# Kernel optimization log

Hardware: AMD Instinct MI355X
Metric: run time of the kernel (lower is better)

Reference implementation:

```python
import math
import jax, jax.numpy as jnp
import numpy as np

B, S, D = 4, 2048, 1024
NEG = -1e20

def setup_inputs() -> dict:
    key = jax.random.key(0)
    k1, k2, k3, k4 = jax.random.split(key, 4)
    X = jax.random.normal(k1, (B, S, D), dtype=jnp.float32)
    # True = masked position (masked_fill semantics)
    attention_mask = jax.random.randint(k2, (B, S, S), 0, 2).astype(bool)
    scale = 1.0 / math.sqrt(D)
    W_qkv = jax.random.normal(k3, (D, 3 * D), dtype=jnp.float32) * scale
    b_qkv = jnp.zeros((3 * D,), dtype=jnp.float32)
    W_out = jax.random.normal(k4, (D, D), dtype=jnp.float32) * scale
    b_out = jnp.zeros((D,), dtype=jnp.float32)
    return {"X": X, "attention_mask": attention_mask,
            "W_qkv": W_qkv, "b_qkv": b_qkv, "W_out": W_out, "b_out": b_out}

def reference(X, attention_mask, W_qkv, b_qkv, W_out, b_out):
    dim = X.shape[-1]
    QKV = X @ W_qkv + b_qkv                      # [B,S,3D]
    Q, K, V = jnp.split(QKV, 3, axis=-1)         # each [B,S,D]
    scores = jnp.einsum('bqd,bkd->bqk', Q, K) / math.sqrt(dim)  # [B,S,S]
    scores = jnp.where(attention_mask, NEG, scores)
    attn = jax.nn.softmax(scores, axis=-1)       # dropout_rate=0.0 -> identity
    ctx = jnp.einsum('bqk,bkd->bqd', attn, V)    # [B,S,D]
    return ctx @ W_out + b_out
```

## Files before the change

### kernel.cpp

```cpp
#include <hip/hip_runtime.h>
#include <cstdint>
#include <cstddef>

#define BB 4
#define SS 2048
#define DD 1024

typedef _Float16 f16;
typedef _Float16 f16x8 __attribute__((ext_vector_type(8)));
typedef _Float16 f16x4 __attribute__((ext_vector_type(4)));
typedef float fx4 __attribute__((ext_vector_type(4)));

__device__ __forceinline__ void async_copy16(void* lds, const void* g) {
  __builtin_amdgcn_global_load_lds(
      (__attribute__((address_space(1))) void*)const_cast<void*>(g),
      (__attribute__((address_space(3))) void*)lds,
      16, 0, 0);
}

enum { EPI_BIAS = 0, EPI_MASKEXP = 1, EPI_ROWSCALE = 2, EPI_QKV = 3 };

template <typename OutT, int MODE>
__global__ __launch_bounds__(256, 2) void gemm_nt(
    const f16* __restrict__ A, long long strideA, int lda,
    const f16* __restrict__ Bt, long long strideB, int ldb,
    OutT* __restrict__ C, long long strideC, int ldc,
    const float* __restrict__ bias, const int* __restrict__ mask,
    float* __restrict__ rowSum, f16* __restrict__ vt, float scale, int K) {
  constexpr int SMEM_BYTES = (MODE == EPI_MASKEXP) ? 34816 : 32768;
  __shared__ __align__(16) char smem[SMEM_BYTES];
  uint32_t* lmb = (uint32_t*)(smem + 32768);

  const int t = threadIdx.x;
  const int lane = t & 63;
  const int wid = t >> 6;
  const long long bz = blockIdx.z;
  const int tileM = blockIdx.y * 128;
  const int tileN = blockIdx.x * 128;

  const f16* Ab = A + bz * strideA;
  const f16* Bb = Bt + bz * strideB;
  OutT* Cb = C + bz * strideC;

  const int sr = t >> 2;
  const int sc = (((t & 3) ^ ((t >> 3) & 3)) * 8);
  const f16* pa0 = Ab + (size_t)(tileM + sr) * lda + sc;
  const f16* pa1 = Ab + (size_t)(tileM + 64 + sr) * lda + sc;
  const f16* pb0 = Bb + (size_t)(tileN + sr) * ldb + sc;
  const f16* pb1 = Bb + (size_t)(tileN + 64 + sr) * ldb + sc;
  const int tb = t * 16;

  const int waveM = (wid >> 1) * 64;
  const int waveN = (wid & 1) * 64;
  const int r16 = lane & 15;
  const int quad = lane >> 4;
  const int sw = (r16 >> 1) & 3;

  if constexpr (MODE == EPI_MASKEXP) {
    const int* maskb = mask + bz * (long long)SS * SS;
#pragma unroll
    for (int it = 0; it < 16; ++it) {
      const int f = it * 256 + t;
      const int4 mv =
          *(const int4*)&maskb[(size_t)(tileM + (f >> 5)) * SS + tileN + (f & 31) * 4];
      uint32_t val = (mv.x ? 1u : 0u) | (mv.y ? 2u : 0u) | (mv.z ? 4u : 0u) |
                     (mv.w ? 8u : 0u);
      val <<= (t & 7) * 4;
      val |= __shfl_xor(val, 1, 64);
      val |= __shfl_xor(val, 2, 64);
      val |= __shfl_xor(val, 4, 64);
      if ((t & 7) == 0) lmb[it * 32 + (t >> 3)] = val;
    }
    __syncthreads();
  }

  const int nIter = K >> 5;
  {
    char* b0 = smem;
    async_copy16(b0 + tb, pa0);
    async_copy16(b0 + 4096 + tb, pa1);
    async_copy16(b0 + 8192 + tb, pb0);
    async_copy16(b0 + 12288 + tb, pb1);
  }

  fx4 acc[4][4] = {};

#pragma unroll 2
  for (int i = 0; i < nIter; ++i) {
    __syncthreads();
    if (i + 1 < nIter) {
      char* nb = smem + ((i + 1) & 1) * 16384;
      const int k = (i + 1) << 5;
      async_copy16(nb + tb, pa0 + k);
      async_copy16(nb + 4096 + tb, pa1 + k);
      async_copy16(nb + 8192 + tb, pb0 + k);
      async_copy16(nb + 12288 + tb, pb1 + k);
    }
    const f16* As = (const f16*)(smem + (i & 1) * 16384);
    const f16* Bs = As + 4096;

    f16x8 af[4], bf[4];
#pragma unroll
    for (int x = 0; x < 4; ++x)
      af[x] = *(const f16x8*)&As[(waveM + x * 16 + r16) * 32 + (quad ^ sw) * 8];
#pragma unroll
    for (int x = 0; x < 4; ++x)
      bf[x] = *(const f16x8*)&Bs[(waveN + x * 16 + r16) * 32 + (quad ^ sw) * 8];

#pragma unroll
    for (int x = 0; x < 4; ++x)
#pragma unroll
      for (int j = 0; j < 4; ++j)
        acc[x][j] =
            __builtin_amdgcn_mfma_f32_16x16x32_f16(af[x], bf[j], acc[x][j], 0, 0, 0);
  }

  if constexpr (MODE == EPI_BIAS) {
#pragma unroll
    for (int j = 0; j < 4; ++j) {
      const int col = tileN + waveN + j * 16 + r16;
      const float bv = bias[col];
#pragma unroll
      for (int i = 0; i < 4; ++i) {
#pragma unroll
        for (int r = 0; r < 4; ++r) {
          const int row = tileM + waveM + i * 16 + quad * 4 + r;
          Cb[(size_t)row * ldc + col] = (OutT)(acc[i][j][r] * scale + bv);
        }
      }
    }
  } else if constexpr (MODE == EPI_QKV) {
    if (tileN < 2 * DD) {
#pragma unroll
      for (int j = 0; j < 4; ++j) {
        const int col = tileN + waveN + j * 16 + r16;
        const float bv = bias[col];
#pragma unroll
        for (int i = 0; i < 4; ++i) {
#pragma unroll
          for (int r = 0; r < 4; ++r) {
            const int row = tileM + waveM + i * 16 + quad * 4 + r;
            Cb[(size_t)row * ldc + col] = (OutT)(acc[i][j][r] + bv);
          }
        }
      }
    } else {
      const int b = tileM >> 11;
      const int s0 = (tileM & 2047) + waveM;
      f16* vb = vt + (size_t)b * DD * SS;
#pragma unroll
      for (int j = 0; j < 4; ++j) {
        const int col = tileN + waveN + j * 16 + r16;
        const float bv = bias[col];
        const int d = col - 2 * DD;
#pragma unroll
        for (int i = 0; i < 4; ++i) {
          const int s = s0 + i * 16 + quad * 4;
          f16x4 v4;
#pragma unroll
          for (int r = 0; r < 4; ++r) v4[r] = (f16)(acc[i][j][r] + bv);
          *(f16x4*)&vb[(size_t)d * SS + s] = v4;
        }
      }
    }
  } else if constexpr (MODE == EPI_MASKEXP) {
#pragma unroll
    for (int i = 0; i < 4; ++i) {
#pragma unroll
      for (int r = 0; r < 4; ++r) {
        const int lr = waveM + i * 16 + quad * 4 + r;
        const int row = tileM + lr;
        const uint32_t w0 = lmb[lr * 4 + (waveN >> 5)];
        const uint32_t w1 = lmb[lr * 4 + (waveN >> 5) + 1];
        float part = 0.0f;
#pragma unroll
        for (int j = 0; j < 4; ++j) {
          const int lc = waveN + j * 16 + r16;
          const int bitpos = j * 16 + r16;
          const uint32_t mv = ((j < 2 ? w0 : w1) >> (bitpos & 31)) & 1u;
          const float e = mv ? 0.0f : __expf(acc[i][j][r] * scale);
          Cb[(size_t)row * ldc + tileN + lc] = (OutT)e;
          part += e;
        }
#pragma unroll
        for (int d = 1; d < 16; d <<= 1) part += __shfl_xor(part, d, 64);
        if (r16 == 0) atomicAdd(&rowSum[bz * SS + row], part);
      }
    }
  } else {
#pragma unroll
    for (int i = 0; i < 4; ++i) {
#pragma unroll
      for (int r = 0; r < 4; ++r) {
        const int row = tileM + waveM + i * 16 + quad * 4 + r;
        const float inv = scale / rowSum[bz * SS + row];
#pragma unroll
        for (int j = 0; j < 4; ++j) {
          const int col = tileN + waveN + j * 16 + r16;
          Cb[(size_t)row * ldc + col] = (OutT)(acc[i][j][r] * inv);
        }
      }
    }
  }
}

__global__ __launch_bounds__(256) void k_prep(
    const float* __restrict__ X, f16* __restrict__ Xh,
    const float* __restrict__ Wqkv, f16* __restrict__ Wqkvt,
    const float* __restrict__ Wout, f16* __restrict__ Woutt,
    float* __restrict__ rowSum) {
  int bid = blockIdx.x;
  const int t = threadIdx.x;
  if (bid < 8192) {
    const int i = bid * 256 + t;
    const float4 v = ((const float4*)X)[i];
    f16x4 h = {(f16)v.x, (f16)v.y, (f16)v.z, (f16)v.w};
    ((f16x4*)Xh)[i] = h;
    return;
  }
  bid -= 8192;
  __shared__ float tile[32][33];
  const int tx = t & 31, ty = t >> 5;
  if (bid < 3072) {
    const int bx = (bid % 96) * 32, by = (bid / 96) * 32;
    for (int i2 = ty; i2 < 32; i2 += 8)
      tile[i2][tx] = Wqkv[(size_t)(by + i2) * 3072 + bx + tx];
    __syncthreads();
    for (int i2 = ty; i2 < 32; i2 += 8)
      Wqkvt[(size_t)(bx + i2) * 1024 + by + tx] = (f16)tile[tx][i2];
    return;
  }
  bid -= 3072;
  if (bid < 1024) {
    const int bx = (bid & 31) * 32, by = (bid >> 5) * 32;
    for (int i2 = ty; i2 < 32; i2 += 8)
      tile[i2][tx] = Wout[(size_t)(by + i2) * 1024 + bx + tx];
    __syncthreads();
    for (int i2 = ty; i2 < 32; i2 += 8)
      Woutt[(size_t)(bx + i2) * 1024 + by + tx] = (f16)tile[tx][i2];
    return;
  }
  bid -= 1024;
  rowSum[bid * 256 + t] = 0.0f;
}

extern "C" void kernel_launch(void* const* d_in, const int* in_sizes, int n_in,
                              void* d_out, int out_size, void* d_ws, size_t ws_size,
                              hipStream_t stream) {
  const float* X = (const float*)d_in[0];
  const int* mask = (const int*)d_in[1];
  const float* Wqkv = (const float*)d_in[2];
  const float* bqkv = (const float*)d_in[3];
  const float* Wout = (const float*)d_in[4];
  const float* bout = (const float*)d_in[5];
  float* out = (float*)d_out;

  char* ws = (char*)d_ws;
  f16* Xh = (f16*)(ws + 0);
  f16* Wqkvt = (f16*)(ws + 16777216);
  f16* Woutt = (f16*)(ws + 23068672);
  f16* QK = (f16*)(ws + 25165824);
  f16* Vt = (f16*)(ws + 58720256);
  f16* E = (f16*)(ws + 75497472);
  f16* Ctx = (f16*)(ws + 109051904);
  float* rowSum = (float*)(ws + 125829120);

  k_prep<<<dim3(12320), dim3(256), 0, stream>>>(X, Xh, Wqkv, Wqkvt, Wout, Woutt,
                                                rowSum);

  gemm_nt<f16, EPI_QKV><<<dim3(24, 64, 1), dim3(256), 0, stream>>>(
      Xh, 0LL, DD, Wqkvt, 0LL, DD, QK, 0LL, 2 * DD, bqkv, nullptr, nullptr, Vt,
      1.0f, DD);

  gemm_nt<f16, EPI_MASKEXP><<<dim3(16, 16, 4), dim3(256), 0, stream>>>(
      QK, (long long)SS * 2 * DD, 2 * DD, QK + DD, (long long)SS * 2 * DD, 2 * DD,
      E, (long long)SS * SS, SS, nullptr, mask, rowSum, nullptr, 0.03125f, DD);

  gemm_nt<f16, EPI_ROWSCALE><<<dim3(8, 16, 4), dim3(256), 0, stream>>>(
      E, (long long)SS * SS, SS, Vt, (long long)DD * SS, SS, Ctx,
      (long long)SS * DD, DD, nullptr, nullptr, rowSum, nullptr, 1.0f, SS);

  gemm_nt<float, EPI_BIAS><<<dim3(8, 64, 1), dim3(256), 0, stream>>>(
      Ctx, 0LL, DD, Woutt, 0LL, DD, out, 0LL, DD, bout, nullptr, nullptr, nullptr,
      1.0f, DD);
}
```

Baseline: 338.2 us.

## Use 256x256 eight-wave GEMM tiles with ping-pong LDS schedule and prepacked mask bits

The GEMM grows from 128x128 tiles with 4 waves to 256x256 tiles with 8 waves. Each wave now holds a 128x64 accumulator, and K-steps of 64 are double-buffered in 128KB of LDS, with explicit barriers, waitcnt and setprio interleaving loads with MFMA bursts. The aim is more data reuse per LDS byte and better overlap of copies with math. The int mask is packed into bitmasks once in the prep kernel, stored in a workspace region that aliases the Ctx buffer, and read directly in the epilogue, so the per-tile mask staging is gone. The risk is that the smaller grids (128 blocks for two of the GEMMs) and one block per CU may leave many CUs idle.

```diff
diff --git a/kernel.cpp b/kernel.cpp
--- a/kernel.cpp
+++ b/kernel.cpp
@@ -21,98 +21,124 @@
 enum { EPI_BIAS = 0, EPI_MASKEXP = 1, EPI_ROWSCALE = 2, EPI_QKV = 3 };
 
 template <typename OutT, int MODE>
-__global__ __launch_bounds__(256, 2) void gemm_nt(
+__global__ __launch_bounds__(512, 2) void gemm_nt8(
     const f16* __restrict__ A, long long strideA, int lda,
     const f16* __restrict__ Bt, long long strideB, int ldb,
     OutT* __restrict__ C, long long strideC, int ldc,
-    const float* __restrict__ bias, const int* __restrict__ mask,
+    const float* __restrict__ bias, const uint32_t* __restrict__ gmask,
     float* __restrict__ rowSum, f16* __restrict__ vt, float scale, int K) {
-  constexpr int SMEM_BYTES = (MODE == EPI_MASKEXP) ? 34816 : 32768;
-  __shared__ __align__(16) char smem[SMEM_BYTES];
-  uint32_t* lmb = (uint32_t*)(smem + 32768);
+  __shared__ __align__(16) char smem[131072];
 
   const int t = threadIdx.x;
   const int lane = t & 63;
   const int wid = t >> 6;
   const long long bz = blockIdx.z;
-  const int tileM = blockIdx.y * 128;
-  const int tileN = blockIdx.x * 128;
+  const int tileM = blockIdx.y * 256;
+  const int tileN = blockIdx.x * 256;
 
   const f16* Ab = A + bz * strideA;
   const f16* Bb = Bt + bz * strideB;
   OutT* Cb = C + bz * strideC;
 
-  const int sr = t >> 2;
-  const int sc = (((t & 3) ^ ((t >> 3) & 3)) * 8);
-  const f16* pa0 = Ab + (size_t)(tileM + sr) * lda + sc;
-  const f16* pa1 = Ab + (size_t)(tileM + 64 + sr) * lda + sc;
-  const f16* pb0 = Bb + (size_t)(tileN + sr) * ldb + sc;
-  const f16* pb1 = Bb + (size_t)(tileN + 64 + sr) * ldb + sc;
+  const int gch = ((t & 3) ^ ((t >> 3) & 3)) * 8;
+  const f16* pA = Ab + (size_t)(tileM + (t >> 2)) * lda + gch;
+  const f16* pB = Bb + (size_t)(tileN + (t >> 2)) * ldb + gch;
+  const size_t rA = (size_t)128 * lda;
+  const size_t rB = (size_t)128 * ldb;
   const int tb = t * 16;
 
-  const int waveM = (wid >> 1) * 64;
-  const int waveN = (wid & 1) * 64;
+  const int waveM = (wid >> 2) * 128;
+  const int waveN = (wid & 3) * 64;
   const int r16 = lane & 15;
   const int quad = lane >> 4;
   const int sw = (r16 >> 1) & 3;
 
-  if constexpr (MODE == EPI_MASKEXP) {
-    const int* maskb = mask + bz * (long long)SS * SS;
-#pragma unroll
-    for (int it = 0; it < 16; ++it) {
-      const int f = it * 256 + t;
-      const int4 mv =
-          *(const int4*)&maskb[(size_t)(tileM + (f >> 5)) * SS + tileN + (f & 31) * 4];
-      uint32_t val = (mv.x ? 1u : 0u) | (mv.y ? 2u : 0u) | (mv.z ? 4u : 0u) |
-                     (mv.w ? 8u : 0u);
-      val <<= (t & 7) * 4;
-      val |= __shfl_xor(val, 1, 64);
-      val |= __shfl_xor(val, 2, 64);
-      val |= __shfl_xor(val, 4, 64);
-      if ((t & 7) == 0) lmb[it * 32 + (t >> 3)] = val;
-    }
-    __syncthreads();
-  }
-
-  const int nIter = K >> 5;
-  {
-    char* b0 = smem;
-    async_copy16(b0 + tb, pa0);
-    async_copy16(b0 + 4096 + tb, pa1);
-    async_copy16(b0 + 8192 + tb, pb0);
-    async_copy16(b0 + 12288 + tb, pb1);
-  }
-
-  fx4 acc[4][4] = {};
-
-#pragma unroll 2
-  for (int i = 0; i < nIter; ++i) {
-    __syncthreads();
-    if (i + 1 < nIter) {
-      char* nb = smem + ((i + 1) & 1) * 16384;
-      const int k = (i + 1) << 5;
-      async_copy16(nb + tb, pa0 + k);
-      async_copy16(nb + 4096 + tb, pa1 + k);
-      async_copy16(nb + 8192 + tb, pb0 + k);
-      async_copy16(nb + 12288 + tb, pb1 + k);
-    }
-    const f16* As = (const f16*)(smem + (i & 1) * 16384);
-    const f16* Bs = As + 4096;
-
-    f16x8 af[4], bf[4];
-#pragma unroll
-    for (int x = 0; x < 4; ++x)
-      af[x] = *(const f16x8*)&As[(waveM + x * 16 + r16) * 32 + (quad ^ sw) * 8];
-#pragma unroll
-    for (int x = 0; x < 4; ++x)
-      bf[x] = *(const f16x8*)&Bs[(waveN + x * 16 + r16) * 32 + (quad ^ sw) * 8];
-
-#pragma unroll
-    for (int x = 0; x < 4; ++x)
-#pragma unroll
-      for (int j = 0; j < 4; ++j)
-        acc[x][j] =
-            __builtin_amdgcn_mfma_f32_16x16x32_f16(af[x], bf[j], acc[x][j], 0, 0, 0);
+  const int nT = K >> 6;
+
+#define STG_A(par, ks, Tn)                                      \
+  {                                                             \
+    char* d_ = smem + (par) * 65536 + (ks) * 16384;             \
+    const f16* s_ = pA + (size_t)(Tn) * 64 + (ks) * 32;         \
+    async_copy16(d_ + tb, s_);                                  \
+    async_copy16(d_ + 8192 + tb, s_ + rA);                      \
+  }
+#define STG_B(par, ks, Tn)                                      \
+  {                                                             \
+    char* d_ = smem + (par) * 65536 + 32768 + (ks) * 16384;     \
+    const f16* s_ = pB + (size_t)(Tn) * 64 + (ks) * 32;         \
+    async_copy16(d_ + tb, s_);                                  \
+    async_copy16(d_ + 8192 + tb, s_ + rB);                      \
+  }
+
+  STG_A(0, 0, 0);
+  STG_B(0, 0, 0);
+  STG_A(0, 1, 0);
+  STG_B(0, 1, 0);
+  asm volatile("s_waitcnt vmcnt(4)" ::: "memory");
+  __builtin_amdgcn_s_barrier();
+  __builtin_amdgcn_sched_barrier(0);
+
+  fx4 acc[8][4] = {};
+  f16x8 af[4], bf[4];
+
+#define LOADB(Bs)                                                              \
+  _Pragma("unroll") for (int j = 0; j < 4; ++j) bf[j] =                        \
+      *(const f16x8*)&(Bs)[(waveN + j * 16 + r16) * 32 + (quad ^ sw) * 8];
+#define LOADA(As, mo)                                                          \
+  _Pragma("unroll") for (int m = 0; m < 4; ++m) af[m] =                        \
+      *(const f16x8*)&(As)[(waveM + (mo) + m * 16 + r16) * 32 + (quad ^ sw) * 8];
+#define MFMA16(mo)                                                             \
+  __builtin_amdgcn_s_setprio(1);                                               \
+  _Pragma("unroll") for (int m = 0; m < 4; ++m)                                \
+  _Pragma("unroll") for (int j = 0; j < 4; ++j)                                \
+      acc[(mo) + m][j] = __builtin_amdgcn_mfma_f32_16x16x32_f16(               \
+          af[m], bf[j], acc[(mo) + m][j], 0, 0, 0);                            \
+  __builtin_amdgcn_s_setprio(0);
+
+  for (int T = 0; T < nT; ++T) {
+    const int par = T & 1;
+    const int np = par ^ 1;
+    const bool st = (T + 1) < nT;
+    const f16* As0 = (const f16*)(smem + par * 65536);
+    const f16* As1 = As0 + 8192;
+    const f16* Bs0 = As0 + 16384;
+    const f16* Bs1 = As0 + 24576;
+
+    LOADB(Bs0);
+    LOADA(As0, 0);
+    if (st) STG_A(np, 0, T + 1);
+    __builtin_amdgcn_s_barrier();
+    MFMA16(0);
+    __builtin_amdgcn_s_barrier();
+
+    LOADA(As0, 64);
+    if (st) STG_B(np, 0, T + 1);
+    __builtin_amdgcn_s_barrier();
+    MFMA16(4);
+    if (st) {
+      asm volatile("s_waitcnt vmcnt(4)" ::: "memory");
+    } else {
+      asm volatile("s_waitcnt vmcnt(0)" ::: "memory");
+    }
+    __builtin_amdgcn_s_barrier();
+    __builtin_amdgcn_sched_barrier(0);
+
+    LOADB(Bs1);
+    LOADA(As1, 0);
+    if (st) STG_A(np, 1, T + 1);
+    __builtin_amdgcn_s_barrier();
+    MFMA16(0);
+    __builtin_amdgcn_s_barrier();
+
+    LOADA(As1, 64);
+    if (st) STG_B(np, 1, T + 1);
+    __builtin_amdgcn_s_barrier();
+    MFMA16(4);
+    if (st) {
+      asm volatile("s_waitcnt vmcnt(4)" ::: "memory");
+    }
+    __builtin_amdgcn_s_barrier();
+    __builtin_amdgcn_sched_barrier(0);
   }
 
   if constexpr (MODE == EPI_BIAS) {
@@ -121,11 +147,11 @@
       const int col = tileN + waveN + j * 16 + r16;
       const float bv = bias[col];
 #pragma unroll
-      for (int i = 0; i < 4; ++i) {
+      for (int m = 0; m < 8; ++m) {
 #pragma unroll
         for (int r = 0; r < 4; ++r) {
-          const int row = tileM + waveM + i * 16 + quad * 4 + r;
-          Cb[(size_t)row * ldc + col] = (OutT)(acc[i][j][r] * scale + bv);
+          const int row = tileM + waveM + m * 16 + quad * 4 + r;
+          Cb[(size_t)row * ldc + col] = (OutT)(acc[m][j][r] * scale + bv);
         }
       }
     }
@@ -136,11 +162,11 @@
         const int col = tileN + waveN + j * 16 + r16;
         const float bv = bias[col];
 #pragma unroll
-        for (int i = 0; i < 4; ++i) {
+        for (int m = 0; m < 8; ++m) {
 #pragma unroll
           for (int r = 0; r < 4; ++r) {
-            const int row = tileM + waveM + i * 16 + quad * 4 + r;
-            Cb[(size_t)row * ldc + col] = (OutT)(acc[i][j][r] + bv);
+            const int row = tileM + waveM + m * 16 + quad * 4 + r;
+            Cb[(size_t)row * ldc + col] = (OutT)(acc[m][j][r] + bv);
           }
         }
       }
@@ -154,32 +180,31 @@
         const float bv = bias[col];
         const int d = col - 2 * DD;
 #pragma unroll
-        for (int i = 0; i < 4; ++i) {
-          const int s = s0 + i * 16 + quad * 4;
+        for (int m = 0; m < 8; ++m) {
+          const int s = s0 + m * 16 + quad * 4;
           f16x4 v4;
 #pragma unroll
-          for (int r = 0; r < 4; ++r) v4[r] = (f16)(acc[i][j][r] + bv);
+          for (int r = 0; r < 4; ++r) v4[r] = (f16)(acc[m][j][r] + bv);
           *(f16x4*)&vb[(size_t)d * SS + s] = v4;
         }
       }
     }
   } else if constexpr (MODE == EPI_MASKEXP) {
 #pragma unroll
-    for (int i = 0; i < 4; ++i) {
+    for (int m = 0; m < 8; ++m) {
 #pragma unroll
       for (int r = 0; r < 4; ++r) {
-        const int lr = waveM + i * 16 + quad * 4 + r;
-        const int row = tileM + lr;
-        const uint32_t w0 = lmb[lr * 4 + (waveN >> 5)];
-        const uint32_t w1 = lmb[lr * 4 + (waveN >> 5) + 1];
+        const int row = tileM + waveM + m * 16 + quad * 4 + r;
+        const uint32_t* gr =
+            gmask + (((size_t)bz * SS + row) << 6) + ((tileN + waveN) >> 5);
+        const uint32_t w0 = gr[0], w1 = gr[1];
         float part = 0.0f;
 #pragma unroll
         for (int j = 0; j < 4; ++j) {
-          const int lc = waveN + j * 16 + r16;
           const int bitpos = j * 16 + r16;
           const uint32_t mv = ((j < 2 ? w0 : w1) >> (bitpos & 31)) & 1u;
-          const float e = mv ? 0.0f : __expf(acc[i][j][r] * scale);
-          Cb[(size_t)row * ldc + tileN + lc] = (OutT)e;
+          const float e = mv ? 0.0f : __expf(acc[m][j][r] * scale);
+          Cb[(size_t)row * ldc + tileN + waveN + j * 16 + r16] = (OutT)e;
           part += e;
         }
 #pragma unroll
@@ -189,26 +214,32 @@
     }
   } else {
 #pragma unroll
-    for (int i = 0; i < 4; ++i) {
+    for (int m = 0; m < 8; ++m) {
 #pragma unroll
       for (int r = 0; r < 4; ++r) {
-        const int row = tileM + waveM + i * 16 + quad * 4 + r;
+        const int row = tileM + waveM + m * 16 + quad * 4 + r;
         const float inv = scale / rowSum[bz * SS + row];
 #pragma unroll
         for (int j = 0; j < 4; ++j) {
           const int col = tileN + waveN + j * 16 + r16;
-          Cb[(size_t)row * ldc + col] = (OutT)(acc[i][j][r] * inv);
-        }
-      }
-    }
-  }
+          Cb[(size_t)row * ldc + col] = (OutT)(acc[m][j][r] * inv);
+        }
+      }
+    }
+  }
+#undef STG_A
+#undef STG_B
+#undef LOADB
+#undef LOADA
+#undef MFMA16
 }
 
 __global__ __launch_bounds__(256) void k_prep(
     const float* __restrict__ X, f16* __restrict__ Xh,
     const float* __restrict__ Wqkv, f16* __restrict__ Wqkvt,
     const float* __restrict__ Wout, f16* __restrict__ Woutt,
-    float* __restrict__ rowSum) {
+    float* __restrict__ rowSum, const int* __restrict__ mask,
+    uint32_t* __restrict__ gmask) {
   int bid = blockIdx.x;
   const int t = threadIdx.x;
   if (bid < 8192) {
@@ -241,7 +272,23 @@
     return;
   }
   bid -= 1024;
-  rowSum[bid * 256 + t] = 0.0f;
+  if (bid < 32) {
+    rowSum[bid * 256 + t] = 0.0f;
+    return;
+  }
+  bid -= 32;
+  const int w = bid * 256 + t;
+  const int4* mr = (const int4*)(mask + ((size_t)w << 5));
+  uint32_t v = 0;
+#pragma unroll
+  for (int c = 0; c < 8; ++c) {
+    const int4 q = mr[c];
+    v |= (q.x ? 1u : 0u) << (c * 4);
+    v |= (q.y ? 1u : 0u) << (c * 4 + 1);
+    v |= (q.z ? 1u : 0u) << (c * 4 + 2);
+    v |= (q.w ? 1u : 0u) << (c * 4 + 3);
+  }
+  gmask[w] = v;
 }
 
 extern "C" void kernel_launch(void* const* d_in, const int* in_sizes, int n_in,
@@ -264,23 +311,24 @@
   f16* E = (f16*)(ws + 75497472);
   f16* Ctx = (f16*)(ws + 109051904);
   float* rowSum = (float*)(ws + 125829120);
-
-  k_prep<<<dim3(12320), dim3(256), 0, stream>>>(X, Xh, Wqkv, Wqkvt, Wout, Woutt,
-                                                rowSum);
-
-  gemm_nt<f16, EPI_QKV><<<dim3(24, 64, 1), dim3(256), 0, stream>>>(
+  uint32_t* gmask = (uint32_t*)(ws + 109051904);
+
+  k_prep<<<dim3(14368), dim3(256), 0, stream>>>(X, Xh, Wqkv, Wqkvt, Wout, Woutt,
+                                                rowSum, mask, gmask);
+
+  gemm_nt8<f16, EPI_QKV><<<dim3(12, 32, 1), dim3(512), 0, stream>>>(
       Xh, 0LL, DD, Wqkvt, 0LL, DD, QK, 0LL, 2 * DD, bqkv, nullptr, nullptr, Vt,
       1.0f, DD);
 
-  gemm_nt<f16, EPI_MASKEXP><<<dim3(16, 16, 4), dim3(256), 0, stream>>>(
+  gemm_nt8<f16, EPI_MASKEXP><<<dim3(8, 8, 4), dim3(512), 0, stream>>>(
       QK, (long long)SS * 2 * DD, 2 * DD, QK + DD, (long long)SS * 2 * DD, 2 * DD,
-      E, (long long)SS * SS, SS, nullptr, mask, rowSum, nullptr, 0.03125f, DD);
-
-  gemm_nt<f16, EPI_ROWSCALE><<<dim3(8, 16, 4), dim3(256), 0, stream>>>(
+      E, (long long)SS * SS, SS, nullptr, gmask, rowSum, nullptr, 0.03125f, DD);
+
+  gemm_nt8<f16, EPI_ROWSCALE><<<dim3(4, 8, 4), dim3(512), 0, stream>>>(
       E, (long long)SS * SS, SS, Vt, (long long)DD * SS, SS, Ctx,
       (long long)SS * DD, DD, nullptr, nullptr, rowSum, nullptr, 1.0f, SS);
 
-  gemm_nt<float, EPI_BIAS><<<dim3(8, 64, 1), dim3(256), 0, stream>>>(
+  gemm_nt8<float, EPI_BIAS><<<dim3(4, 32, 1), dim3(512), 0, stream>>>(
       Ctx, 0LL, DD, Woutt, 0LL, DD, out, 0LL, DD, bout, nullptr, nullptr, nullptr,
       1.0f, DD);
 }
```

New measurement: 372.4 us. 1.1x slower.

## Switch GEMMs to single-wave 64x128 tiles with XCD-aware block remap and packed mask

Applied to the files above, without the earlier changes.

Rewrites the GEMM kernel so each workgroup is one 64-lane wave computing a 64x128 tile. Loads are double-buffered and ordered by explicit vmcnt waits instead of block barriers. Block IDs are remapped so contiguous tiles land on the same XCD chiplet. The attention mask is bit-packed once in the prep kernel into a global buffer, replacing per-tile mask packing in the score GEMM. This trades the 4-wave 128x128 tile's LDS reuse for fewer barriers and more independent workgroups; the packed mask reuses the Ctx workspace region before Ctx is written.

```diff
diff --git a/kernel.cpp b/kernel.cpp
--- a/kernel.cpp
+++ b/kernel.cpp
@@ -21,165 +21,151 @@
 enum { EPI_BIAS = 0, EPI_MASKEXP = 1, EPI_ROWSCALE = 2, EPI_QKV = 3 };
 
 template <typename OutT, int MODE>
-__global__ __launch_bounds__(256, 2) void gemm_nt(
+__global__ __launch_bounds__(64, 2) void gemm_w1(
     const f16* __restrict__ A, long long strideA, int lda,
     const f16* __restrict__ Bt, long long strideB, int ldb,
     OutT* __restrict__ C, long long strideC, int ldc,
-    const float* __restrict__ bias, const int* __restrict__ mask,
-    float* __restrict__ rowSum, f16* __restrict__ vt, float scale, int K) {
-  constexpr int SMEM_BYTES = (MODE == EPI_MASKEXP) ? 34816 : 32768;
-  __shared__ __align__(16) char smem[SMEM_BYTES];
-  uint32_t* lmb = (uint32_t*)(smem + 32768);
-
-  const int t = threadIdx.x;
-  const int lane = t & 63;
-  const int wid = t >> 6;
-  const long long bz = blockIdx.z;
-  const int tileM = blockIdx.y * 128;
-  const int tileN = blockIdx.x * 128;
+    const float* __restrict__ bias, const uint32_t* __restrict__ gmask,
+    float* __restrict__ rowSum, f16* __restrict__ vt, float scale, int K,
+    int gx, int gy) {
+  __shared__ __align__(16) char smem[24576];
+
+  const int lane = threadIdx.x;
+
+  const int nwg = gridDim.x;
+  const int chunk = nwg >> 3;
+  const int bid = blockIdx.x;
+  const int wk = (bid & 7) * chunk + (bid >> 3);
+  const int x = wk % gx;
+  const int yz = wk / gx;
+  const int y = yz % gy;
+  const long long bz = yz / gy;
+
+  const int tileM = y * 64;
+  const int tileN = x * 128;
 
   const f16* Ab = A + bz * strideA;
   const f16* Bb = Bt + bz * strideB;
   OutT* Cb = C + bz * strideC;
 
-  const int sr = t >> 2;
-  const int sc = (((t & 3) ^ ((t >> 3) & 3)) * 8);
-  const f16* pa0 = Ab + (size_t)(tileM + sr) * lda + sc;
-  const f16* pa1 = Ab + (size_t)(tileM + 64 + sr) * lda + sc;
-  const f16* pb0 = Bb + (size_t)(tileN + sr) * ldb + sc;
-  const f16* pb1 = Bb + (size_t)(tileN + 64 + sr) * ldb + sc;
-  const int tb = t * 16;
-
-  const int waveM = (wid >> 1) * 64;
-  const int waveN = (wid & 1) * 64;
+  const int gch = ((lane & 3) ^ ((lane >> 3) & 3)) * 8;
+  const int rl = lane >> 2;
+  const f16* pA = Ab + (size_t)(tileM + rl) * lda + gch;
+  const f16* pB = Bb + (size_t)(tileN + rl) * ldb + gch;
+  const int tb = lane * 16;
+
+#define STG(p, kk)                                                     \
+  {                                                                    \
+    char* dA_ = smem + (p) * 12288;                                    \
+    _Pragma("unroll") for (int j = 0; j < 4; ++j)                      \
+        async_copy16(dA_ + j * 1024 + tb,                              \
+                     pA + (kk) + (size_t)j * 16 * lda);                \
+    char* dB_ = dA_ + 4096;                                            \
+    _Pragma("unroll") for (int j = 0; j < 8; ++j)                      \
+        async_copy16(dB_ + j * 1024 + tb,                              \
+                     pB + (kk) + (size_t)j * 16 * ldb);                \
+  }
+
   const int r16 = lane & 15;
   const int quad = lane >> 4;
   const int sw = (r16 >> 1) & 3;
-
-  if constexpr (MODE == EPI_MASKEXP) {
-    const int* maskb = mask + bz * (long long)SS * SS;
-#pragma unroll
-    for (int it = 0; it < 16; ++it) {
-      const int f = it * 256 + t;
-      const int4 mv =
-          *(const int4*)&maskb[(size_t)(tileM + (f >> 5)) * SS + tileN + (f & 31) * 4];
-      uint32_t val = (mv.x ? 1u : 0u) | (mv.y ? 2u : 0u) | (mv.z ? 4u : 0u) |
-                     (mv.w ? 8u : 0u);
-      val <<= (t & 7) * 4;
-      val |= __shfl_xor(val, 1, 64);
-      val |= __shfl_xor(val, 2, 64);
-      val |= __shfl_xor(val, 4, 64);
-      if ((t & 7) == 0) lmb[it * 32 + (t >> 3)] = val;
-    }
-    __syncthreads();
-  }
+  const int foff = r16 * 32 + (quad ^ sw) * 8;
 
   const int nIter = K >> 5;
-  {
-    char* b0 = smem;
-    async_copy16(b0 + tb, pa0);
-    async_copy16(b0 + 4096 + tb, pa1);
-    async_copy16(b0 + 8192 + tb, pb0);
-    async_copy16(b0 + 12288 + tb, pb1);
-  }
-
-  fx4 acc[4][4] = {};
-
-#pragma unroll 2
+
+  STG(0, 0);
+
+  fx4 acc[4][8] = {};
+
   for (int i = 0; i < nIter; ++i) {
-    __syncthreads();
     if (i + 1 < nIter) {
-      char* nb = smem + ((i + 1) & 1) * 16384;
-      const int k = (i + 1) << 5;
-      async_copy16(nb + tb, pa0 + k);
-      async_copy16(nb + 4096 + tb, pa1 + k);
-      async_copy16(nb + 8192 + tb, pb0 + k);
-      async_copy16(nb + 12288 + tb, pb1 + k);
-    }
-    const f16* As = (const f16*)(smem + (i & 1) * 16384);
-    const f16* Bs = As + 4096;
-
-    f16x8 af[4], bf[4];
-#pragma unroll
-    for (int x = 0; x < 4; ++x)
-      af[x] = *(const f16x8*)&As[(waveM + x * 16 + r16) * 32 + (quad ^ sw) * 8];
-#pragma unroll
-    for (int x = 0; x < 4; ++x)
-      bf[x] = *(const f16x8*)&Bs[(waveN + x * 16 + r16) * 32 + (quad ^ sw) * 8];
-
-#pragma unroll
-    for (int x = 0; x < 4; ++x)
-#pragma unroll
-      for (int j = 0; j < 4; ++j)
-        acc[x][j] =
-            __builtin_amdgcn_mfma_f32_16x16x32_f16(af[x], bf[j], acc[x][j], 0, 0, 0);
-  }
+      STG((i + 1) & 1, (i + 1) << 5);
+      asm volatile("s_waitcnt vmcnt(12)" ::: "memory");
+    } else {
+      asm volatile("s_waitcnt vmcnt(0)" ::: "memory");
+    }
+    __builtin_amdgcn_sched_barrier(0);
+
+    const f16* As = (const f16*)(smem + (i & 1) * 12288);
+    const f16* Bs = As + 2048;
+
+    f16x8 af[4];
+#pragma unroll
+    for (int m = 0; m < 4; ++m) af[m] = *(const f16x8*)&As[m * 512 + foff];
+#pragma unroll
+    for (int n = 0; n < 8; ++n) {
+      const f16x8 bfn = *(const f16x8*)&Bs[n * 512 + foff];
+#pragma unroll
+      for (int m = 0; m < 4; ++m)
+        acc[m][n] =
+            __builtin_amdgcn_mfma_f32_16x16x32_f16(af[m], bfn, acc[m][n], 0, 0, 0);
+    }
+  }
+#undef STG
 
   if constexpr (MODE == EPI_BIAS) {
 #pragma unroll
-    for (int j = 0; j < 4; ++j) {
-      const int col = tileN + waveN + j * 16 + r16;
+    for (int n = 0; n < 8; ++n) {
+      const int col = tileN + n * 16 + r16;
       const float bv = bias[col];
 #pragma unroll
-      for (int i = 0; i < 4; ++i) {
+      for (int m = 0; m < 4; ++m) {
 #pragma unroll
         for (int r = 0; r < 4; ++r) {
-          const int row = tileM + waveM + i * 16 + quad * 4 + r;
-          Cb[(size_t)row * ldc + col] = (OutT)(acc[i][j][r] * scale + bv);
+          const int row = tileM + m * 16 + quad * 4 + r;
+          Cb[(size_t)row * ldc + col] = (OutT)(acc[m][n][r] * scale + bv);
         }
       }
     }
   } else if constexpr (MODE == EPI_QKV) {
     if (tileN < 2 * DD) {
 #pragma unroll
-      for (int j = 0; j < 4; ++j) {
-        const int col = tileN + waveN + j * 16 + r16;
+      for (int n = 0; n < 8; ++n) {
+        const int col = tileN + n * 16 + r16;
         const float bv = bias[col];
 #pragma unroll
-        for (int i = 0; i < 4; ++i) {
+        for (int m = 0; m < 4; ++m) {
 #pragma unroll
           for (int r = 0; r < 4; ++r) {
-            const int row = tileM + waveM + i * 16 + quad * 4 + r;
-            Cb[(size_t)row * ldc + col] = (OutT)(acc[i][j][r] + bv);
+            const int row = tileM + m * 16 + quad * 4 + r;
+            Cb[(size_t)row * ldc + col] = (OutT)(acc[m][n][r] + bv);
           }
         }
       }
     } else {
       const int b = tileM >> 11;
-      const int s0 = (tileM & 2047) + waveM;
+      const int s0 = tileM & 2047;
       f16* vb = vt + (size_t)b * DD * SS;
 #pragma unroll
-      for (int j = 0; j < 4; ++j) {
-        const int col = tileN + waveN + j * 16 + r16;
+      for (int n = 0; n < 8; ++n) {
+        const int col = tileN + n * 16 + r16;
         const float bv = bias[col];
         const int d = col - 2 * DD;
 #pragma unroll
-        for (int i = 0; i < 4; ++i) {
-          const int s = s0 + i * 16 + quad * 4;
+        for (int m = 0; m < 4; ++m) {
+          const int s = s0 + m * 16 + quad * 4;
           f16x4 v4;
 #pragma unroll
-          for (int r = 0; r < 4; ++r) v4[r] = (f16)(acc[i][j][r] + bv);
+          for (int r = 0; r < 4; ++r) v4[r] = (f16)(acc[m][n][r] + bv);
           *(f16x4*)&vb[(size_t)d * SS + s] = v4;
         }
       }
     }
   } else if constexpr (MODE == EPI_MASKEXP) {
 #pragma unroll
-    for (int i = 0; i < 4; ++i) {
+    for (int m = 0; m < 4; ++m) {
 #pragma unroll
       for (int r = 0; r < 4; ++r) {
-        const int lr = waveM + i * 16 + quad * 4 + r;
-        const int row = tileM + lr;
-        const uint32_t w0 = lmb[lr * 4 + (waveN >> 5)];
-        const uint32_t w1 = lmb[lr * 4 + (waveN >> 5) + 1];
+        const int row = tileM + m * 16 + quad * 4 + r;
+        const uint4 g4 = *(const uint4*)(gmask + (((size_t)bz * SS + row) << 6) +
+                                         (tileN >> 5));
         float part = 0.0f;
 #pragma unroll
-        for (int j = 0; j < 4; ++j) {
-          const int lc = waveN + j * 16 + r16;
-          const int bitpos = j * 16 + r16;
-          const uint32_t mv = ((j < 2 ? w0 : w1) >> (bitpos & 31)) & 1u;
-          const float e = mv ? 0.0f : __expf(acc[i][j][r] * scale);
-          Cb[(size_t)row * ldc + tileN + lc] = (OutT)e;
+        for (int n = 0; n < 8; ++n) {
+          const uint32_t w = ((const uint32_t*)&g4)[n >> 1];
+          const uint32_t mv = (w >> ((n & 1) * 16 + r16)) & 1u;
+          const float e = mv ? 0.0f : __expf(acc[m][n][r] * scale);
+          Cb[(size_t)row * ldc + tileN + n * 16 + r16] = (OutT)e;
           part += e;
         }
 #pragma unroll
@@ -189,15 +175,15 @@
     }
   } else {
 #pragma unroll
-    for (int i = 0; i < 4; ++i) {
+    for (int m = 0; m < 4; ++m) {
 #pragma unroll
       for (int r = 0; r < 4; ++r) {
-        const int row = tileM + waveM + i * 16 + quad * 4 + r;
+        const int row = tileM + m * 16 + quad * 4 + r;
         const float inv = scale / rowSum[bz * SS + row];
 #pragma unroll
-        for (int j = 0; j < 4; ++j) {
-          const int col = tileN + waveN + j * 16 + r16;
-          Cb[(size_t)row * ldc + col] = (OutT)(acc[i][j][r] * inv);
+        for (int n = 0; n < 8; ++n) {
+          const int col = tileN + n * 16 + r16;
+          Cb[(size_t)row * ldc + col] = (OutT)(acc[m][n][r] * inv);
         }
       }
     }
@@ -208,7 +194,8 @@
     const float* __restrict__ X, f16* __restrict__ Xh,
     const float* __restrict__ Wqkv, f16* __restrict__ Wqkvt,
     const float* __restrict__ Wout, f16* __restrict__ Woutt,
-    float* __restrict__ rowSum) {
+    float* __restrict__ rowSum, const int* __restrict__ mask,
+    uint32_t* __restrict__ gmask) {
   int bid = blockIdx.x;
   const int t = threadIdx.x;
   if (bid < 8192) {
@@ -241,7 +228,23 @@
     return;
   }
   bid -= 1024;
-  rowSum[bid * 256 + t] = 0.0f;
+  if (bid < 32) {
+    rowSum[bid * 256 + t] = 0.0f;
+    return;
+  }
+  bid -= 32;
+  const int w = bid * 256 + t;
+  const int4* mr = (const int4*)(mask + ((size_t)w << 5));
+  uint32_t v = 0;
+#pragma unroll
+  for (int c = 0; c < 8; ++c) {
+    const int4 q = mr[c];
+    v |= (q.x ? 1u : 0u) << (c * 4);
+    v |= (q.y ? 1u : 0u) << (c * 4 + 1);
+    v |= (q.z ? 1u : 0u) << (c * 4 + 2);
+    v |= (q.w ? 1u : 0u) << (c * 4 + 3);
+  }
+  gmask[w] = v;
 }
 
 extern "C" void kernel_launch(void* const* d_in, const int* in_sizes, int n_in,
@@ -264,23 +267,26 @@
   f16* E = (f16*)(ws + 75497472);
   f16* Ctx = (f16*)(ws + 109051904);
   float* rowSum = (float*)(ws + 125829120);
-
-  k_prep<<<dim3(12320), dim3(256), 0, stream>>>(X, Xh, Wqkv, Wqkvt, Wout, Woutt,
-                                                rowSum);
-
-  gemm_nt<f16, EPI_QKV><<<dim3(24, 64, 1), dim3(256), 0, stream>>>(
+  uint32_t* gmask = (uint32_t*)(ws + 109051904);
+
+  k_prep<<<dim3(14368), dim3(256), 0, stream>>>(X, Xh, Wqkv, Wqkvt, Wout, Woutt,
+                                                rowSum, mask, gmask);
+
+  gemm_w1<f16, EPI_QKV><<<dim3(3072), dim3(64), 0, stream>>>(
       Xh, 0LL, DD, Wqkvt, 0LL, DD, QK, 0LL, 2 * DD, bqkv, nullptr, nullptr, Vt,
-      1.0f, DD);
-
-  gemm_nt<f16, EPI_MASKEXP><<<dim3(16, 16, 4), dim3(256), 0, stream>>>(
+      1.0f, DD, 24, 128);
+
+  gemm_w1<f16, EPI_MASKEXP><<<dim3(2048), dim3(64), 0, stream>>>(
       QK, (long long)SS * 2 * DD, 2 * DD, QK + DD, (long long)SS * 2 * DD, 2 * DD,
-      E, (long long)SS * SS, SS, nullptr, mask, rowSum, nullptr, 0.03125f, DD);
-
-  gemm_nt<f16, EPI_ROWSCALE><<<dim3(8, 16, 4), dim3(256), 0, stream>>>(
+      E, (long long)SS * SS, SS, nullptr, gmask, rowSum, nullptr, 0.03125f, DD,
+      16, 32);
+
+  gemm_w1<f16, EPI_ROWSCALE><<<dim3(1024), dim3(64), 0, stream>>>(
       E, (long long)SS * SS, SS, Vt, (long long)DD * SS, SS, Ctx,
-      (long long)SS * DD, DD, nullptr, nullptr, rowSum, nullptr, 1.0f, SS);
-
-  gemm_nt<float, EPI_BIAS><<<dim3(8, 64, 1), dim3(256), 0, stream>>>(
+      (long long)SS * DD, DD, nullptr, nullptr, rowSum, nullptr, 1.0f, SS,
+      8, 32);
+
+  gemm_w1<float, EPI_BIAS><<<dim3(1024), dim3(64), 0, stream>>>(
       Ctx, 0LL, DD, Woutt, 0LL, DD, out, 0LL, DD, bout, nullptr, nullptr, nullptr,
-      1.0f, DD);
-}
+      1.0f, DD, 8, 128);
+}
```

Result: slower. 389.9 us (+15.3%).

## Triple-buffer GEMM k-loop and precompute packed mask bits in prep kernel

Applied to the files above, without the earlier changes.

Switches the GEMM main loop from double to triple buffering in LDS. It uses explicit vmcnt waits and a single barrier per iteration, so global-to-LDS loads run two stages ahead of the MFMA work. The mask-to-bitmask packing moves out of the score GEMM prologue into the prep kernel, which writes a packed bitmap into workspace that the epilogue reads directly from global memory. LDS grows to 48KB per block, which may reduce occupancy. The bitmap reuses the Ctx workspace region, which is safe only because Ctx is written after the score GEMM has consumed it.

```diff
diff --git a/kernel.cpp b/kernel.cpp
--- a/kernel.cpp
+++ b/kernel.cpp
@@ -25,11 +25,9 @@
     const f16* __restrict__ A, long long strideA, int lda,
     const f16* __restrict__ Bt, long long strideB, int ldb,
     OutT* __restrict__ C, long long strideC, int ldc,
-    const float* __restrict__ bias, const int* __restrict__ mask,
+    const float* __restrict__ bias, const uint32_t* __restrict__ gmask,
     float* __restrict__ rowSum, f16* __restrict__ vt, float scale, int K) {
-  constexpr int SMEM_BYTES = (MODE == EPI_MASKEXP) ? 34816 : 32768;
-  __shared__ __align__(16) char smem[SMEM_BYTES];
-  uint32_t* lmb = (uint32_t*)(smem + 32768);
+  __shared__ __align__(16) char smem[49152];
 
   const int t = threadIdx.x;
   const int lane = t & 63;
@@ -56,47 +54,34 @@
   const int quad = lane >> 4;
   const int sw = (r16 >> 1) & 3;
 
-  if constexpr (MODE == EPI_MASKEXP) {
-    const int* maskb = mask + bz * (long long)SS * SS;
-#pragma unroll
-    for (int it = 0; it < 16; ++it) {
-      const int f = it * 256 + t;
-      const int4 mv =
-          *(const int4*)&maskb[(size_t)(tileM + (f >> 5)) * SS + tileN + (f & 31) * 4];
-      uint32_t val = (mv.x ? 1u : 0u) | (mv.y ? 2u : 0u) | (mv.z ? 4u : 0u) |
-                     (mv.w ? 8u : 0u);
-      val <<= (t & 7) * 4;
-      val |= __shfl_xor(val, 1, 64);
-      val |= __shfl_xor(val, 2, 64);
-      val |= __shfl_xor(val, 4, 64);
-      if ((t & 7) == 0) lmb[it * 32 + (t >> 3)] = val;
-    }
-    __syncthreads();
-  }
-
   const int nIter = K >> 5;
-  {
-    char* b0 = smem;
-    async_copy16(b0 + tb, pa0);
-    async_copy16(b0 + 4096 + tb, pa1);
-    async_copy16(b0 + 8192 + tb, pb0);
-    async_copy16(b0 + 12288 + tb, pb1);
-  }
+
+#define STG(buf, kk)                              \
+  {                                               \
+    char* nb_ = smem + (buf) * 16384;             \
+    async_copy16(nb_ + tb, pa0 + (kk));           \
+    async_copy16(nb_ + 4096 + tb, pa1 + (kk));    \
+    async_copy16(nb_ + 8192 + tb, pb0 + (kk));    \
+    async_copy16(nb_ + 12288 + tb, pb1 + (kk));   \
+  }
+
+  STG(0, 0);
+  STG(1, 32);
 
   fx4 acc[4][4] = {};
 
-#pragma unroll 2
+#pragma unroll 3
   for (int i = 0; i < nIter; ++i) {
-    __syncthreads();
     if (i + 1 < nIter) {
-      char* nb = smem + ((i + 1) & 1) * 16384;
-      const int k = (i + 1) << 5;
-      async_copy16(nb + tb, pa0 + k);
-      async_copy16(nb + 4096 + tb, pa1 + k);
-      async_copy16(nb + 8192 + tb, pb0 + k);
-      async_copy16(nb + 12288 + tb, pb1 + k);
-    }
-    const f16* As = (const f16*)(smem + (i & 1) * 16384);
+      asm volatile("s_waitcnt vmcnt(4)" ::: "memory");
+    } else {
+      asm volatile("s_waitcnt vmcnt(0)" ::: "memory");
+    }
+    __builtin_amdgcn_s_barrier();
+    __builtin_amdgcn_sched_barrier(0);
+    if (i + 2 < nIter) STG((i + 2) % 3, (i + 2) << 5);
+
+    const f16* As = (const f16*)(smem + (i % 3) * 16384);
     const f16* Bs = As + 4096;
 
     f16x8 af[4], bf[4];
@@ -114,6 +99,7 @@
         acc[x][j] =
             __builtin_amdgcn_mfma_f32_16x16x32_f16(af[x], bf[j], acc[x][j], 0, 0, 0);
   }
+#undef STG
 
   if constexpr (MODE == EPI_BIAS) {
 #pragma unroll
@@ -168,18 +154,17 @@
     for (int i = 0; i < 4; ++i) {
 #pragma unroll
       for (int r = 0; r < 4; ++r) {
-        const int lr = waveM + i * 16 + quad * 4 + r;
-        const int row = tileM + lr;
-        const uint32_t w0 = lmb[lr * 4 + (waveN >> 5)];
-        const uint32_t w1 = lmb[lr * 4 + (waveN >> 5) + 1];
+        const int row = tileM + waveM + i * 16 + quad * 4 + r;
+        const uint32_t* gr =
+            gmask + (((size_t)bz * SS + row) << 6) + ((tileN + waveN) >> 5);
+        const uint32_t w0 = gr[0], w1 = gr[1];
         float part = 0.0f;
 #pragma unroll
         for (int j = 0; j < 4; ++j) {
-          const int lc = waveN + j * 16 + r16;
           const int bitpos = j * 16 + r16;
           const uint32_t mv = ((j < 2 ? w0 : w1) >> (bitpos & 31)) & 1u;
           const float e = mv ? 0.0f : __expf(acc[i][j][r] * scale);
-          Cb[(size_t)row * ldc + tileN + lc] = (OutT)e;
+          Cb[(size_t)row * ldc + tileN + waveN + j * 16 + r16] = (OutT)e;
           part += e;
         }
 #pragma unroll
@@ -208,7 +193,8 @@
     const float* __restrict__ X, f16* __restrict__ Xh,
     const float* __restrict__ Wqkv, f16* __restrict__ Wqkvt,
     const float* __restrict__ Wout, f16* __restrict__ Woutt,
-    float* __restrict__ rowSum) {
+    float* __restrict__ rowSum, const int* __restrict__ mask,
+    uint32_t* __restrict__ gmask) {
   int bid = blockIdx.x;
   const int t = threadIdx.x;
   if (bid < 8192) {
@@ -241,7 +227,23 @@
     return;
   }
   bid -= 1024;
-  rowSum[bid * 256 + t] = 0.0f;
+  if (bid < 32) {
+    rowSum[bid * 256 + t] = 0.0f;
+    return;
+  }
+  bid -= 32;
+  const int w = bid * 256 + t;
+  const int4* mr = (const int4*)(mask + ((size_t)w << 5));
+  uint32_t v = 0;
+#pragma unroll
+  for (int c = 0; c < 8; ++c) {
+    const int4 q = mr[c];
+    v |= (q.x ? 1u : 0u) << (c * 4);
+    v |= (q.y ? 1u : 0u) << (c * 4 + 1);
+    v |= (q.z ? 1u : 0u) << (c * 4 + 2);
+    v |= (q.w ? 1u : 0u) << (c * 4 + 3);
+  }
+  gmask[w] = v;
 }
 
 extern "C" void kernel_launch(void* const* d_in, const int* in_sizes, int n_in,
@@ -264,9 +266,10 @@
   f16* E = (f16*)(ws + 75497472);
   f16* Ctx = (f16*)(ws + 109051904);
   float* rowSum = (float*)(ws + 125829120);
-
-  k_prep<<<dim3(12320), dim3(256), 0, stream>>>(X, Xh, Wqkv, Wqkvt, Wout, Woutt,
-                                                rowSum);
+  uint32_t* gmask = (uint32_t*)(ws + 109051904);
+
+  k_prep<<<dim3(14368), dim3(256), 0, stream>>>(X, Xh, Wqkv, Wqkvt, Wout, Woutt,
+                                                rowSum, mask, gmask);
 
   gemm_nt<f16, EPI_QKV><<<dim3(24, 64, 1), dim3(256), 0, stream>>>(
       Xh, 0LL, DD, Wqkvt, 0LL, DD, QK, 0LL, 2 * DD, bqkv, nullptr, nullptr, Vt,
@@ -274,7 +277,7 @@
 
   gemm_nt<f16, EPI_MASKEXP><<<dim3(16, 16, 4), dim3(256), 0, stream>>>(
       QK, (long long)SS * 2 * DD, 2 * DD, QK + DD, (long long)SS * 2 * DD, 2 * DD,
-      E, (long long)SS * SS, SS, nullptr, mask, rowSum, nullptr, 0.03125f, DD);
+      E, (long long)SS * SS, SS, nullptr, gmask, rowSum, nullptr, 0.03125f, DD);
 
   gemm_nt<f16, EPI_ROWSCALE><<<dim3(8, 16, 4), dim3(256), 0, stream>>>(
       E, (long long)SS * SS, SS, Vt, (long long)DD * SS, SS, Ctx,
```

Measured after the change: 347.5 us. +2.8%, slower.
